# Performance work log

Hardware: AMD Instinct MI355X
Metric: run time of the kernel (lower is better)

Reference implementation:

```python
import jax, jax.numpy as jnp
import numpy as np

EPS = 1e-8


def _l2_normalize(x, eps=EPS):
    n = jnp.linalg.norm(x, axis=-1, keepdims=True)
    return x / jnp.maximum(n, eps)


def setup_inputs() -> dict:
    key = jax.random.key(0)
    k1, k2, k3 = jax.random.split(key, 3)
    N_s, N_q, D, C = 65536, 131072, 256, 512
    return {
        "support_features": jax.random.normal(k1, (N_s, D), dtype=jnp.float32),
        "support_labels": jax.random.randint(k2, (N_s,), 0, C, dtype=jnp.int64),
        "query_features": jax.random.normal(k3, (N_q, D), dtype=jnp.float32),
        "logit_scale": jnp.asarray(5.0, dtype=jnp.float32),
        "proto_shrink": jnp.asarray(-2.0, dtype=jnp.float32),
        "num_classes": C,
    }


def reference(support_features, support_labels, query_features, logit_scale, proto_shrink, num_classes):
    # L2-normalize features
    s = _l2_normalize(support_features)            # [N_s, D]
    q = _l2_normalize(query_features)              # [N_q, D]

    labels = support_labels.astype(jnp.int32)
    # per-class segment mean (replaces the python unique/mask loop)
    sums = jax.ops.segment_sum(s, labels, num_segments=num_classes)        # [C, D]
    counts = jax.ops.segment_sum(jnp.ones((s.shape[0],), s.dtype), labels,
                                 num_segments=num_classes)                 # [C]
    counts = jnp.maximum(counts, 1.0)
    class_means = sums / counts[:, None]                                   # [C, D]

    global_centroid = jnp.mean(s, axis=0, keepdims=True)                    # [1, D]

    alpha_base = jnp.clip(jax.nn.sigmoid(proto_shrink), 0.0, 0.4)
    alpha = (alpha_base / jnp.sqrt(counts))[:, None]                        # [C, 1]
    prototypes = (1.0 - alpha) * class_means + alpha * global_centroid
    prototypes = _l2_normalize(prototypes)                                  # [C, D]

    scale = jnp.clip(logit_scale, 1.0, 100.0)
    logits = q @ prototypes.T * scale                                       # [N_q, C]
    unique_classes = jnp.arange(num_classes, dtype=jnp.int32)
    return logits, unique_classes
```

## Files before the change

### kernel.cpp

```cpp
#include <hip/hip_runtime.h>

typedef __attribute__((ext_vector_type(4)))  float f32x4;
typedef __attribute__((ext_vector_type(16))) float f32x16;
typedef __attribute__((ext_vector_type(8)))  short short8;

#define DD 256
#define CC 512
#define LDP2 264

__device__ __forceinline__ unsigned short f2bf(float f) {
    union { float f; unsigned u; } x; x.f = f;
    unsigned r = x.u + 0x7FFFu + ((x.u >> 16) & 1u);
    return (unsigned short)(r >> 16);
}

__device__ __forceinline__ f32x4 ntload4(const f32x4* p) {
    return __builtin_nontemporal_load(p);
}

__global__ __launch_bounds__(256) void class_sum_kernel(
    const f32x4* __restrict__ S, const int* __restrict__ labels,
    float* __restrict__ sums2, float* __restrict__ counts2, int N_s)
{
    const int c = blockIdx.x >> 1, half = blockIdx.x & 1;
    const int w = threadIdx.x >> 6, l = threadIdx.x & 63;
    const int seg  = N_s >> 3;
    const int base = half * (N_s >> 1) + w * seg;
    const int4* lab4 = (const int4*)(labels + base);
    const int iters = seg >> 8;

    float ax = 0.f, ay = 0.f, az = 0.f, aw = 0.f;
    int cnt = 0;

    int4 pf0 = lab4[l];
    int4 pf1 = (iters > 1) ? lab4[64 + l] : make_int4(-1, -1, -1, -1);

    for (int it = 0; it < iters; ++it) {
        int4 lv = pf0;
        pf0 = pf1;
        pf1 = (it + 2 < iters) ? lab4[(it + 2) * 64 + l] : make_int4(-1, -1, -1, -1);
        #pragma unroll
        for (int s = 0; s < 4; ++s) {
            int lab = (s == 0) ? lv.x : (s == 1) ? lv.y : (s == 2) ? lv.z : lv.w;
            unsigned long long m = __ballot(lab == c);
            cnt += __popcll(m);
            while (m) {
                int p0 = __ffsll((long long)m) - 1; m &= m - 1;
                int p1 = -1, p2 = -1, p3 = -1;
                if (m) { p1 = __ffsll((long long)m) - 1; m &= m - 1;
                    if (m) { p2 = __ffsll((long long)m) - 1; m &= m - 1;
                        if (m) { p3 = __ffsll((long long)m) - 1; m &= m - 1; } } }
                f32x4 v0 = ntload4(&S[(size_t)(base + (it * 64 + p0) * 4 + s) * 64 + l]);
                f32x4 v1 = {0,0,0,0}, v2 = {0,0,0,0}, v3 = {0,0,0,0};
                if (p1 >= 0) v1 = ntload4(&S[(size_t)(base + (it * 64 + p1) * 4 + s) * 64 + l]);
                if (p2 >= 0) v2 = ntload4(&S[(size_t)(base + (it * 64 + p2) * 4 + s) * 64 + l]);
                if (p3 >= 0) v3 = ntload4(&S[(size_t)(base + (it * 64 + p3) * 4 + s) * 64 + l]);
                float s0 = v0[0]*v0[0] + v0[1]*v0[1] + v0[2]*v0[2] + v0[3]*v0[3];
                float s1 = v1[0]*v1[0] + v1[1]*v1[1] + v1[2]*v1[2] + v1[3]*v1[3];
                float s2 = v2[0]*v2[0] + v2[1]*v2[1] + v2[2]*v2[2] + v2[3]*v2[3];
                float s3 = v3[0]*v3[0] + v3[1]*v3[1] + v3[2]*v3[2] + v3[3]*v3[3];
                #pragma unroll
                for (int off = 32; off; off >>= 1) {
                    s0 += __shfl_xor(s0, off);
                    s1 += __shfl_xor(s1, off);
                    s2 += __shfl_xor(s2, off);
                    s3 += __shfl_xor(s3, off);
                }
                float i0 = 1.0f / fmaxf(sqrtf(s0), 1e-8f);
                ax += v0[0]*i0; ay += v0[1]*i0; az += v0[2]*i0; aw += v0[3]*i0;
                if (p1 >= 0) { float i1 = 1.0f / fmaxf(sqrtf(s1), 1e-8f);
                    ax += v1[0]*i1; ay += v1[1]*i1; az += v1[2]*i1; aw += v1[3]*i1; }
                if (p2 >= 0) { float i2 = 1.0f / fmaxf(sqrtf(s2), 1e-8f);
                    ax += v2[0]*i2; ay += v2[1]*i2; az += v2[2]*i2; aw += v2[3]*i2; }
                if (p3 >= 0) { float i3 = 1.0f / fmaxf(sqrtf(s3), 1e-8f);
                    ax += v3[0]*i3; ay += v3[1]*i3; az += v3[2]*i3; aw += v3[3]*i3; }
            }
        }
    }

    __shared__ float lred[4][DD];
    __shared__ float lcnt[4];
    lred[w][4*l+0] = ax; lred[w][4*l+1] = ay; lred[w][4*l+2] = az; lred[w][4*l+3] = aw;
    if (l == 0) lcnt[w] = (float)cnt;
    __syncthreads();
    int t = threadIdx.x;
    sums2[(size_t)(half * CC + c) * DD + t] = lred[0][t] + lred[1][t] + lred[2][t] + lred[3][t];
    if (t == 0) counts2[half * CC + c] = lcnt[0] + lcnt[1] + lcnt[2] + lcnt[3];
}

__global__ __launch_bounds__(256) void centroid_kernel(
    const float* __restrict__ sums2, float* __restrict__ gpart)
{
    const int d = threadIdx.x, b = blockIdx.x;
    float s = 0.f;
    for (int j = 0; j < 64; ++j) {
        int c = b * 64 + j;
        s += sums2[(size_t)c * DD + d] + sums2[(size_t)(CC + c) * DD + d];
    }
    gpart[b * DD + d] = s;
}

__global__ __launch_bounds__(256) void proto_kernel(
    const float* __restrict__ sums2, const float* __restrict__ counts2,
    const float* __restrict__ gpart, const float* __restrict__ proto_shrink,
    unsigned short* __restrict__ Pt, float* __restrict__ outUC, int N_s)
{
    const int c = blockIdx.x, d = threadIdx.x;
    float ps = proto_shrink[0];
    float ab = 1.0f / (1.0f + __expf(-ps));
    ab = fminf(fmaxf(ab, 0.0f), 0.4f);

    float sum  = sums2[(size_t)c * DD + d] + sums2[(size_t)(CC + c) * DD + d];
    float cntv = fmaxf(counts2[c] + counts2[CC + c], 1.0f);
    float g = 0.f;
    #pragma unroll
    for (int b = 0; b < 8; ++b) g += gpart[b * DD + d];
    g /= (float)N_s;

    float mean  = sum / cntv;
    float alpha = ab / sqrtf(cntv);
    float p = (1.0f - alpha) * mean + alpha * g;

    float ss = p * p;
    #pragma unroll
    for (int off = 32; off; off >>= 1) ss += __shfl_xor(ss, off);
    __shared__ float l4[4];
    if ((threadIdx.x & 63) == 0) l4[threadIdx.x >> 6] = ss;
    __syncthreads();
    ss = l4[0] + l4[1] + l4[2] + l4[3];
    float inv = 1.0f / fmaxf(sqrtf(ss), 1e-8f);

    const int CT = c >> 5, KT = d >> 4;
    const int lane = (c & 31) + 32 * ((d >> 3) & 1);
    const int e = d & 7;
    Pt[(size_t)(((CT * 16 + KT) * 64 + lane)) * 8 + e] = f2bf(p * inv);
    if (d == 0) outUC[c] = (float)c;
}

__global__ __launch_bounds__(512, 2) void logits_kernel(
    const float4* __restrict__ Q, const unsigned short* __restrict__ Pt,
    const float* __restrict__ logit_scale, float* __restrict__ out, int nch)
{
    __shared__ unsigned short A[2][32 * LDP2];

    const int t  = threadIdx.x;
    const int w  = t >> 6, l = t & 63;
    const int lr = l & 31, lh = l >> 5;
    const int m0 = blockIdx.x * nch * 32;
    const int sr = t >> 4, sc = t & 15;

    const float s = fminf(fmaxf(logit_scale[0], 1.0f), 100.0f);

    short8 b[32];
    #pragma unroll
    for (int ct = 0; ct < 2; ++ct)
        #pragma unroll
        for (int k = 0; k < 16; ++k)
            b[ct * 16 + k] = *(const short8*)(Pt + (size_t)(((2 * w + ct) * 16 + k) * 64 + l) * 8);

    float4 v[4];
    const float4* qbase = Q + ((size_t)(m0 + sr) * DD + sc * 16) / 4;

    #pragma unroll
    for (int i = 0; i < 4; ++i) v[i] = qbase[i];
    {
        float ss = 0.f;
        #pragma unroll
        for (int i = 0; i < 4; ++i)
            ss += v[i].x*v[i].x + v[i].y*v[i].y + v[i].z*v[i].z + v[i].w*v[i].w;
        ss += __shfl_xor(ss, 1); ss += __shfl_xor(ss, 2);
        ss += __shfl_xor(ss, 4); ss += __shfl_xor(ss, 8);
        float inv = 1.0f / fmaxf(sqrtf(ss), 1e-8f);
        unsigned short* dst = &A[0][sr * LDP2 + sc * 16];
        #pragma unroll
        for (int h = 0; h < 2; ++h) {
            short8 pk;
            float4 x = v[2*h], y = v[2*h+1];
            pk[0] = (short)f2bf(x.x*inv); pk[1] = (short)f2bf(x.y*inv);
            pk[2] = (short)f2bf(x.z*inv); pk[3] = (short)f2bf(x.w*inv);
            pk[4] = (short)f2bf(y.x*inv); pk[5] = (short)f2bf(y.y*inv);
            pk[6] = (short)f2bf(y.z*inv); pk[7] = (short)f2bf(y.w*inv);
            *(short8*)(dst + h * 8) = pk;
        }
    }
    if (nch > 1) {
        const float4* src = qbase + 32 * (DD / 4);
        #pragma unroll
        for (int i = 0; i < 4; ++i) v[i] = src[i];
    }
    __builtin_amdgcn_sched_barrier(0);
    asm volatile("s_waitcnt lgkmcnt(0)");
    __builtin_amdgcn_sched_barrier(0);
    __builtin_amdgcn_s_barrier();
    __builtin_amdgcn_sched_barrier(0);

    for (int c = 0; c < nch; ++c) {
        const int p = c & 1;
        f32x16 acc0, acc1;
        #pragma unroll
        for (int r = 0; r < 16; ++r) { acc0[r] = 0.f; acc1[r] = 0.f; }
        const unsigned short* ab = &A[p][lr * LDP2 + lh * 8];
        __builtin_amdgcn_s_setprio(1);
        #pragma unroll
        for (int k = 0; k < 16; ++k) {
            short8 af = *(const short8*)(ab + k * 16);
            acc0 = __builtin_amdgcn_mfma_f32_32x32x16_bf16(af, b[k],      acc0, 0, 0, 0);
            acc1 = __builtin_amdgcn_mfma_f32_32x32x16_bf16(af, b[k + 16], acc1, 0, 0, 0);
        }
        __builtin_amdgcn_s_setprio(0);
        {
            const int col  = 64 * w + lr;
            const int rb   = m0 + c * 32 + 4 * lh;
            #pragma unroll
            for (int r = 0; r < 16; ++r) {
                int row = rb + (r & 3) + 8 * (r >> 2);
                __builtin_nontemporal_store(acc0[r] * s, &out[(size_t)row * CC + col]);
                __builtin_nontemporal_store(acc1[r] * s, &out[(size_t)row * CC + col + 32]);
            }
        }
        __builtin_amdgcn_sched_barrier(0);
        asm volatile("s_waitcnt lgkmcnt(0)");
        __builtin_amdgcn_sched_barrier(0);
        __builtin_amdgcn_s_barrier();
        __builtin_amdgcn_sched_barrier(0);

        if (c + 1 < nch) {
            float ss = 0.f;
            #pragma unroll
            for (int i = 0; i < 4; ++i)
                ss += v[i].x*v[i].x + v[i].y*v[i].y + v[i].z*v[i].z + v[i].w*v[i].w;
            ss += __shfl_xor(ss, 1); ss += __shfl_xor(ss, 2);
            ss += __shfl_xor(ss, 4); ss += __shfl_xor(ss, 8);
            float inv = 1.0f / fmaxf(sqrtf(ss), 1e-8f);
            unsigned short* dst = &A[p ^ 1][sr * LDP2 + sc * 16];
            #pragma unroll
            for (int h = 0; h < 2; ++h) {
                short8 pk;
                float4 x = v[2*h], y = v[2*h+1];
                pk[0] = (short)f2bf(x.x*inv); pk[1] = (short)f2bf(x.y*inv);
                pk[2] = (short)f2bf(x.z*inv); pk[3] = (short)f2bf(x.w*inv);
                pk[4] = (short)f2bf(y.x*inv); pk[5] = (short)f2bf(y.y*inv);
                pk[6] = (short)f2bf(y.z*inv); pk[7] = (short)f2bf(y.w*inv);
                *(short8*)(dst + h * 8) = pk;
            }
            if (c + 2 < nch) {
                const float4* src = qbase + (size_t)(c + 2) * 32 * (DD / 4);
                #pragma unroll
                for (int i = 0; i < 4; ++i) v[i] = src[i];
            }
            __builtin_amdgcn_sched_barrier(0);
            asm volatile("s_waitcnt lgkmcnt(0)");
            __builtin_amdgcn_sched_barrier(0);
            __builtin_amdgcn_s_barrier();
            __builtin_amdgcn_sched_barrier(0);
        }
    }
}

extern "C" void kernel_launch(void* const* d_in, const int* in_sizes, int n_in,
                              void* d_out, int out_size, void* d_ws, size_t ws_size,
                              hipStream_t stream) {
    const float* S      = (const float*)d_in[0];
    const int*   labels = (const int*)d_in[1];
    const float* Qf     = (const float*)d_in[2];
    const float* lscale = (const float*)d_in[3];
    const float* pshr   = (const float*)d_in[4];

    const int N_s = in_sizes[0] / DD;
    const int N_q = in_sizes[2] / DD;

    float* sums2         = (float*)d_ws;
    float* counts2       = (float*)((char*)d_ws + 1048576);
    float* gpart         = (float*)((char*)d_ws + 1052672);
    unsigned short* Pt   = (unsigned short*)((char*)d_ws + 1060864);

    float* out   = (float*)d_out;
    float* outUC = out + (size_t)N_q * CC;

    const int nblk = 256;
    const int nch  = N_q / (nblk * 32);

    class_sum_kernel<<<2 * CC, 256, 0, stream>>>((const f32x4*)S, labels, sums2, counts2, N_s);
    centroid_kernel<<<8, 256, 0, stream>>>(sums2, gpart);
    proto_kernel<<<CC, 256, 0, stream>>>(sums2, counts2, gpart, pshr, Pt, outUC, N_s);
    logits_kernel<<<nblk, 512, 0, stream>>>((const float4*)Qf, Pt, lscale, out, nch);
}
```

Before: 111.6 us.

## Double query chunk to 64 rows, fold logit scale into prototypes, single barrier

Each block now normalizes and stages 64 query rows per chunk instead of 32. Each thread loads 8 float4s, and the loop runs two 32-row MFMA sub-tiles per chunk. The next chunk's normalization and staging now happen before the MFMAs rather than after, so there is one barrier per chunk instead of two. The logit scale is multiplied into the bf16 prototypes, which removes the per-element multiply in the store loop but rounds the scale into the bf16 values. LDS use per block doubles and register pressure rises from the larger v[] array, which could hurt occupancy under the 2-blocks-per-CU launch bounds.

```diff
diff --git a/kernel.cpp b/kernel.cpp
--- a/kernel.cpp
+++ b/kernel.cpp
@@ -103,12 +103,14 @@
 __global__ __launch_bounds__(256) void proto_kernel(
     const float* __restrict__ sums2, const float* __restrict__ counts2,
     const float* __restrict__ gpart, const float* __restrict__ proto_shrink,
+    const float* __restrict__ logit_scale,
     unsigned short* __restrict__ Pt, float* __restrict__ outUC, int N_s)
 {
     const int c = blockIdx.x, d = threadIdx.x;
     float ps = proto_shrink[0];
     float ab = 1.0f / (1.0f + __expf(-ps));
     ab = fminf(fmaxf(ab, 0.0f), 0.4f);
+    const float sc = fminf(fmaxf(logit_scale[0], 1.0f), 100.0f);
 
     float sum  = sums2[(size_t)c * DD + d] + sums2[(size_t)(CC + c) * DD + d];
     float cntv = fmaxf(counts2[c] + counts2[CC + c], 1.0f);
@@ -128,7 +130,7 @@
     if ((threadIdx.x & 63) == 0) l4[threadIdx.x >> 6] = ss;
     __syncthreads();
     ss = l4[0] + l4[1] + l4[2] + l4[3];
-    float inv = 1.0f / fmaxf(sqrtf(ss), 1e-8f);
+    float inv = sc / fmaxf(sqrtf(ss), 1e-8f);
 
     const int CT = c >> 5, KT = d >> 4;
     const int lane = (c & 31) + 32 * ((d >> 3) & 1);
@@ -139,17 +141,15 @@
 
 __global__ __launch_bounds__(512, 2) void logits_kernel(
     const float4* __restrict__ Q, const unsigned short* __restrict__ Pt,
-    const float* __restrict__ logit_scale, float* __restrict__ out, int nch)
-{
-    __shared__ unsigned short A[2][32 * LDP2];
+    float* __restrict__ out, int nch)
+{
+    __shared__ unsigned short A[2][64 * LDP2];
 
     const int t  = threadIdx.x;
     const int w  = t >> 6, l = t & 63;
     const int lr = l & 31, lh = l >> 5;
-    const int m0 = blockIdx.x * nch * 32;
-    const int sr = t >> 4, sc = t & 15;
-
-    const float s = fminf(fmaxf(logit_scale[0], 1.0f), 100.0f);
+    const int m0 = blockIdx.x * nch * 64;
+    const int sr = t >> 3, sc = t & 7;
 
     short8 b[32];
     #pragma unroll
@@ -158,22 +158,22 @@
         for (int k = 0; k < 16; ++k)
             b[ct * 16 + k] = *(const short8*)(Pt + (size_t)(((2 * w + ct) * 16 + k) * 64 + l) * 8);
 
-    float4 v[4];
-    const float4* qbase = Q + ((size_t)(m0 + sr) * DD + sc * 16) / 4;
-
-    #pragma unroll
-    for (int i = 0; i < 4; ++i) v[i] = qbase[i];
+    const float4* qbase = Q + (size_t)(m0 + sr) * 64 + sc * 8;
+
+    float4 v[8];
+    #pragma unroll
+    for (int i = 0; i < 8; ++i) v[i] = qbase[i];
+
     {
         float ss = 0.f;
         #pragma unroll
-        for (int i = 0; i < 4; ++i)
+        for (int i = 0; i < 8; ++i)
             ss += v[i].x*v[i].x + v[i].y*v[i].y + v[i].z*v[i].z + v[i].w*v[i].w;
-        ss += __shfl_xor(ss, 1); ss += __shfl_xor(ss, 2);
-        ss += __shfl_xor(ss, 4); ss += __shfl_xor(ss, 8);
+        ss += __shfl_xor(ss, 1); ss += __shfl_xor(ss, 2); ss += __shfl_xor(ss, 4);
         float inv = 1.0f / fmaxf(sqrtf(ss), 1e-8f);
-        unsigned short* dst = &A[0][sr * LDP2 + sc * 16];
-        #pragma unroll
-        for (int h = 0; h < 2; ++h) {
+        unsigned short* dst = &A[0][sr * LDP2 + sc * 32];
+        #pragma unroll
+        for (int h = 0; h < 4; ++h) {
             short8 pk;
             float4 x = v[2*h], y = v[2*h+1];
             pk[0] = (short)f2bf(x.x*inv); pk[1] = (short)f2bf(x.y*inv);
@@ -184,9 +184,9 @@
         }
     }
     if (nch > 1) {
-        const float4* src = qbase + 32 * (DD / 4);
-        #pragma unroll
-        for (int i = 0; i < 4; ++i) v[i] = src[i];
+        const float4* src = qbase + (size_t)64 * 64;
+        #pragma unroll
+        for (int i = 0; i < 8; ++i) v[i] = src[i];
     }
     __builtin_amdgcn_sched_barrier(0);
     asm volatile("s_waitcnt lgkmcnt(0)");
@@ -196,45 +196,17 @@
 
     for (int c = 0; c < nch; ++c) {
         const int p = c & 1;
-        f32x16 acc0, acc1;
-        #pragma unroll
-        for (int r = 0; r < 16; ++r) { acc0[r] = 0.f; acc1[r] = 0.f; }
-        const unsigned short* ab = &A[p][lr * LDP2 + lh * 8];
-        __builtin_amdgcn_s_setprio(1);
-        #pragma unroll
-        for (int k = 0; k < 16; ++k) {
-            short8 af = *(const short8*)(ab + k * 16);
-            acc0 = __builtin_amdgcn_mfma_f32_32x32x16_bf16(af, b[k],      acc0, 0, 0, 0);
-            acc1 = __builtin_amdgcn_mfma_f32_32x32x16_bf16(af, b[k + 16], acc1, 0, 0, 0);
-        }
-        __builtin_amdgcn_s_setprio(0);
-        {
-            const int col  = 64 * w + lr;
-            const int rb   = m0 + c * 32 + 4 * lh;
-            #pragma unroll
-            for (int r = 0; r < 16; ++r) {
-                int row = rb + (r & 3) + 8 * (r >> 2);
-                __builtin_nontemporal_store(acc0[r] * s, &out[(size_t)row * CC + col]);
-                __builtin_nontemporal_store(acc1[r] * s, &out[(size_t)row * CC + col + 32]);
-            }
-        }
-        __builtin_amdgcn_sched_barrier(0);
-        asm volatile("s_waitcnt lgkmcnt(0)");
-        __builtin_amdgcn_sched_barrier(0);
-        __builtin_amdgcn_s_barrier();
-        __builtin_amdgcn_sched_barrier(0);
 
         if (c + 1 < nch) {
             float ss = 0.f;
             #pragma unroll
-            for (int i = 0; i < 4; ++i)
+            for (int i = 0; i < 8; ++i)
                 ss += v[i].x*v[i].x + v[i].y*v[i].y + v[i].z*v[i].z + v[i].w*v[i].w;
-            ss += __shfl_xor(ss, 1); ss += __shfl_xor(ss, 2);
-            ss += __shfl_xor(ss, 4); ss += __shfl_xor(ss, 8);
+            ss += __shfl_xor(ss, 1); ss += __shfl_xor(ss, 2); ss += __shfl_xor(ss, 4);
             float inv = 1.0f / fmaxf(sqrtf(ss), 1e-8f);
-            unsigned short* dst = &A[p ^ 1][sr * LDP2 + sc * 16];
-            #pragma unroll
-            for (int h = 0; h < 2; ++h) {
+            unsigned short* dst = &A[p ^ 1][sr * LDP2 + sc * 32];
+            #pragma unroll
+            for (int h = 0; h < 4; ++h) {
                 short8 pk;
                 float4 x = v[2*h], y = v[2*h+1];
                 pk[0] = (short)f2bf(x.x*inv); pk[1] = (short)f2bf(x.y*inv);
@@ -244,16 +216,41 @@
                 *(short8*)(dst + h * 8) = pk;
             }
             if (c + 2 < nch) {
-                const float4* src = qbase + (size_t)(c + 2) * 32 * (DD / 4);
+                const float4* src = qbase + (size_t)(c + 2) * 64 * 64;
                 #pragma unroll
-                for (int i = 0; i < 4; ++i) v[i] = src[i];
-            }
-            __builtin_amdgcn_sched_barrier(0);
-            asm volatile("s_waitcnt lgkmcnt(0)");
-            __builtin_amdgcn_sched_barrier(0);
-            __builtin_amdgcn_s_barrier();
-            __builtin_amdgcn_sched_barrier(0);
-        }
+                for (int i = 0; i < 8; ++i) v[i] = src[i];
+            }
+        }
+
+        #pragma unroll
+        for (int st = 0; st < 2; ++st) {
+            f32x16 acc0, acc1;
+            #pragma unroll
+            for (int r = 0; r < 16; ++r) { acc0[r] = 0.f; acc1[r] = 0.f; }
+            const unsigned short* ab = &A[p][(st * 32 + lr) * LDP2 + lh * 8];
+            __builtin_amdgcn_s_setprio(1);
+            #pragma unroll
+            for (int k = 0; k < 16; ++k) {
+                short8 af = *(const short8*)(ab + k * 16);
+                acc0 = __builtin_amdgcn_mfma_f32_32x32x16_bf16(af, b[k],      acc0, 0, 0, 0);
+                acc1 = __builtin_amdgcn_mfma_f32_32x32x16_bf16(af, b[k + 16], acc1, 0, 0, 0);
+            }
+            __builtin_amdgcn_s_setprio(0);
+            const int col = 64 * w + lr;
+            const int rb  = m0 + c * 64 + st * 32 + 4 * lh;
+            #pragma unroll
+            for (int r = 0; r < 16; ++r) {
+                int row = rb + (r & 3) + 8 * (r >> 2);
+                __builtin_nontemporal_store(acc0[r], &out[(size_t)row * CC + col]);
+                __builtin_nontemporal_store(acc1[r], &out[(size_t)row * CC + col + 32]);
+            }
+        }
+
+        __builtin_amdgcn_sched_barrier(0);
+        asm volatile("s_waitcnt lgkmcnt(0)");
+        __builtin_amdgcn_sched_barrier(0);
+        __builtin_amdgcn_s_barrier();
+        __builtin_amdgcn_sched_barrier(0);
     }
 }
 
@@ -278,10 +275,10 @@
     float* outUC = out + (size_t)N_q * CC;
 
     const int nblk = 256;
-    const int nch  = N_q / (nblk * 32);
+    const int nch  = N_q / (nblk * 64);
 
     class_sum_kernel<<<2 * CC, 256, 0, stream>>>((const f32x4*)S, labels, sums2, counts2, N_s);
     centroid_kernel<<<8, 256, 0, stream>>>(sums2, gpart);
-    proto_kernel<<<CC, 256, 0, stream>>>(sums2, counts2, gpart, pshr, Pt, outUC, N_s);
-    logits_kernel<<<nblk, 512, 0, stream>>>((const float4*)Qf, Pt, lscale, out, nch);
-}
+    proto_kernel<<<CC, 256, 0, stream>>>(sums2, counts2, gpart, pshr, lscale, Pt, outUC, N_s);
+    logits_kernel<<<nblk, 512, 0, stream>>>((const float4*)Qf, Pt, out, nch);
+}
```

Result: no change. 110.6 us (-0.9%).
